# Optimization experiments

Hardware: AMD Instinct MI355X
Metric: run time of the kernel (lower is better)

## Reference

```python
import jax, jax.numpy as jnp
import numpy as np

# (dx, dy) per TL_table order: lower_right, down, lower_left, right, left, upper_right, up, upper_left
DIRS = [(1, 1), (0, 1), (-1, 1), (1, 0), (-1, 0), (1, -1), (0, -1), (-1, -1)]


def shift(x, dr, dc, pad=0.0):
    # result[r, c] = x[r - dr, c - dc]; out-of-range filled with `pad`.
    B, R, C = x.shape
    pr = (dr, 0) if dr >= 0 else (0, -dr)
    pc = (dc, 0) if dc >= 0 else (0, -dc)
    y = jnp.pad(x, ((0, 0), pr, pc), constant_values=pad)
    r0 = 0 if dr >= 0 else -dr
    c0 = 0 if dc >= 0 else -dc
    return y[:, r0:r0 + R, c0:c0 + C]


def conn_mask_gen(mask, K):
    m = mask[:, 0]  # [B, R, C]
    # conn[i] = mask * mask shifted by K pixels in direction DIRS[i]
    return jnp.stack([m * shift(m, K * dy, K * dx) for (dx, dy) in DIRS], axis=1)


def get_zero_one_mask(mask, K):
    inv = 1.0 - mask[:, 0]  # [B, R, C]
    inv_static = jnp.broadcast_to(inv[:, None], (inv.shape[0], 8) + inv.shape[1:])
    # inverse_direction_mask is initialized to ONES -> shift with pad=1, reversed direction
    inv_dir = jnp.stack([shift(inv, -K * dy, -K * dx, pad=1.0) for (dx, dy) in DIRS], axis=1)
    return inv_static * (1.0 - inv_static * inv_dir)


def pair_loss(c_map, conn_mask, K, positive):
    c = c_map[:, 0]  # [B, R, C]
    p1 = conn_mask * c[:, None]  # [B, 8, R, C]
    # p2[i] = (conn_mask[7-i] * c) shifted K pixels in direction DIRS[i]
    p2 = jnp.stack([shift(conn_mask[:, 7 - i] * c, K * dy, K * dx)
                    for i, (dx, dy) in enumerate(DIRS)], axis=1)
    pp = p1 * p2
    if positive:
        term1 = conn_mask * (-jnp.log(p2 + 1e-4) - jnp.log(p1 + 1e-4))
        term2 = conn_mask * (-jnp.log(pp + 1e-4) + jnp.exp(-pp))
    else:
        term1 = conn_mask * (-jnp.log(1.0 - p2 + 1e-4) - jnp.log(1.0 - p1 + 1e-4))
        term2 = conn_mask * (-jnp.log(1.0 - pp + 1e-4) + jnp.exp(-pp))
    return conn_mask * term1 / (term2 + 1e-5)


def neighbor_loss(c_map, target, T1, T2, K):
    zom = get_zero_one_mask(target, K)  # [B, 8, R, C]
    c = c_map[:, 0]
    p2 = jnp.stack([shift(zom[:, i] * c, K * dy, K * dx)
                    for i, (dx, dy) in enumerate(DIRS)], axis=1)
    p1m = jnp.stack([shift(zom[:, i], K * dy, K * dx)
                     for i, (dx, dy) in enumerate(DIRS)], axis=1)
    p1 = p1m * c[:, None]
    term1 = -T1 * p1m * jnp.log(1.0 - p2 + 1e-4) - T2 * p1m * jnp.log(p1 + 1e-5)
    term2 = -p1m * jnp.log(1.0 - p1 * p2 + 1e-4) + p1m * jnp.exp(-p2)
    return (p1m * term1 / (term2 + 1e-5)).mean()


def sc_loss(c_map, target_f):
    c = jax.nn.sigmoid(c_map)
    nb1 = neighbor_loss(c, target_f, 0.8, 0.2, K=1)
    nb2 = neighbor_loss(c, target_f, 0.8, 0.2, K=2)
    n1 = pair_loss(c, conn_mask_gen(1.0 - target_f, 1), 1, positive=False)
    n2 = pair_loss(c, conn_mask_gen(1.0 - target_f, 2), 2, positive=False)
    p1 = pair_loss(c, conn_mask_gen(target_f, 1), 1, positive=True)
    p2 = pair_loss(c, conn_mask_gen(target_f, 2), 2, positive=True)
    loss = 0.7 * (n1 + 0.5 * n2) + 0.3 * (p1 + 0.5 * p2) + 0.7 * (0.5 * nb1 + 0.5 * nb2)
    return loss.mean()


def setup_inputs() -> dict:
    key = jax.random.key(0)
    k1, k2 = jax.random.split(key)
    B, H, W = 8, 512, 512
    c_map = jax.random.normal(k1, (B, 1, H, W), dtype=jnp.float32)
    target = jax.random.randint(k2, (B, 1, H, W), 0, 2, dtype=jnp.int32)
    return {"c_map": c_map, "target": target}


def reference(c_map, target):
    return sc_loss(c_map, target.astype(jnp.float32))
```

## Files before the change

kernel.cpp:

```cpp
#include <hip/hip_runtime.h>

#define IMG_H 512
#define IMG_W 512
#define NB    8
#define TILE  32
#define LROWS 34
#define LCOLS 36
#define NBLK  (NB * (IMG_H / TILE) * (IMG_W / TILE))
#define N_MEAN 16777216.0
#define LOG2E 1.44269504f
#define LN2   0.69314718f

__device__ __forceinline__ float frcp(float x){ return __builtin_amdgcn_rcpf(x); }
__device__ __forceinline__ float fexp2(float x){ return __builtin_amdgcn_exp2f(x); }
__device__ __forceinline__ float flog2(float x){ return __builtin_amdgcn_logf(x); }

__global__ __launch_bounds__(256) void scloss_main(
    const float* __restrict__ cmap, const int* __restrict__ tgt,
    float* __restrict__ partials)
{
    __shared__ float4 pack[LROWS * LCOLS];

    const int tilesPerRow = IMG_W / TILE;
    const int tilesPerImg = (IMG_H / TILE) * tilesPerRow;
    int blk = blockIdx.x;
    int b   = blk / tilesPerImg;
    int ti  = blk % tilesPerImg;
    int tr  = (ti / tilesPerRow) * TILE;
    int tc  = (ti % tilesPerRow) * TILE;

    const float* cimg = cmap + (size_t)b * (IMG_H * IMG_W);
    const int*   timg = tgt  + (size_t)b * (IMG_H * IMG_W);

    for (int idx = threadIdx.x; idx < LROWS * LCOLS; idx += 256) {
        int lr = idx / LCOLS, lc = idx - lr * LCOLS;
        int gr = tr + lr, gc = tc + lc - 2;
        float4 v = make_float4(0.0f, 0.0f, 0.0f, 0.0f);
        if (gr < IMG_H && (unsigned)gc < (unsigned)IMG_W) {
            float x = cimg[gr * IMG_W + gc];
            bool  t = timg[gr * IMG_W + gc] != 0;
            float s   = frcp(1.0f + fexp2(x * -LOG2E));
            float sel = t ? s : (1.0f - s);
            float L   = LN2 * flog2(sel + 1e-4f);
            float e   = fexp2(s * -LOG2E);
            v = make_float4(s,
                            (t ? -0.6f : -1.4f) * L,
                            t ? -e : e,
                            (t ? -0.07f : -0.28f) * L);
        }
        pack[idx] = v;
    }
    __syncthreads();

    int j  = threadIdx.x & 31;
    int i0 = threadIdx.x >> 5;
    float acc = 0.0f;

#define EDGE(VBX, Dd, Nn, WSK, MK) do {                                   \
        float4 vb  = (VBX);                                               \
        bool  tb   = vb.z < 0.0f;                                         \
        bool  qpos = (ta == tb);                  \
        bool  qnz  = vb.z != 0.0f;                \
        float ppp  = __builtin_fmaf(sa, vb.x, 1e-4f);                     \
        float ompp = __builtin_fmaf(-sa, vb.x, 1.0001f);                  \
        float argc = (qpos && ta) ? ppp : ompp;                           \
        float lg   = flog2(argc);                                         \
        float E    = fexp2(__builtin_fmaf(ppp, -LOG2E, 1e-4f * LOG2E));   \
        float een  = ta ? vb.z : epa;         \
        float ee   = qpos ? E : een;                                      \
        Dd         = __builtin_fmaf(-LN2, lg, ee);                        \
        float nm   = qpos ? __builtin_fmaf(WSK, vb.y, MK) : (nwa + vb.w); \
        Nn         = qnz ? nm : 0.0f;                                     \
    } while (0)

#define COMBINE do {                                                      \
        float d01 = D0 * D1, d23 = D2 * D3;                               \
        float R   = frcp(d01 * d23);                                      \
        float n01 = __builtin_fmaf(N1, D0, N0 * D1);                      \
        float n23 = __builtin_fmaf(N3, D2, N2 * D3);                      \
        acc = __builtin_fmaf(__builtin_fmaf(n23, d01, n01 * d23), R, acc);\
    } while (0)

#define PIXEL(VA, S1X, S2X, base) do {                                    \
        float4 va_ = (VA);                                                \
        bool  ta  = va_.z < 0.0f;                                         \
        float sa  = va_.x, nwa = va_.w, epa = va_.z;                      \
        float mwa = va_.y, hmw = 0.5f * va_.y;                            \
        float D0, D1, D2, D3, N0, N1, N2, N3;                             \
        EDGE(base[1],           D0, N0, 1.0f, mwa);            \
        EDGE(base[LCOLS + 1],   D1, N1, 1.0f, mwa);            \
        EDGE(S1X,               D2, N2, 1.0f, mwa);            \
        EDGE(base[LCOLS - 1],   D3, N3, 1.0f, mwa);            \
        COMBINE;                                                          \
        EDGE(base[2],           D0, N0, 0.5f, hmw);            \
        EDGE(base[2*LCOLS + 2], D1, N1, 0.5f, hmw);            \
        EDGE(S2X,               D2, N2, 0.5f, hmw);            \
        EDGE(base[2*LCOLS - 2], D3, N3, 0.5f, hmw);            \
        COMBINE;                                                          \
    } while (0)

    {
        const float4* b0 = &pack[(i0 * 4) * LCOLS + (j + 2)];
        const float4* b1 = b0 + LCOLS;
        const float4* b2 = b1 + LCOLS;
        const float4* b3 = b2 + LCOLS;
        float4 va0 = b0[0], va1 = b1[0], va2 = b2[0], va3 = b3[0];
        PIXEL(va0, va1, va2,            b0);
        PIXEL(va1, va2, va3,            b1);
        PIXEL(va2, va3, b2[2 * LCOLS],  b2);
        PIXEL(va3, b3[LCOLS], b3[2 * LCOLS], b3);
    }
#undef PIXEL
#undef COMBINE
#undef EDGE

    #pragma unroll
    for (int o = 32; o > 0; o >>= 1) acc += __shfl_down(acc, o, 64);
    __shared__ float wsum[4];
    int lane = threadIdx.x & 63, wid = threadIdx.x >> 6;
    if (lane == 0) wsum[wid] = acc;
    __syncthreads();
    if (threadIdx.x == 0)
        partials[blockIdx.x] = wsum[0] + wsum[1] + wsum[2] + wsum[3];
}

__global__ __launch_bounds__(256) void scloss_final(
    const float* __restrict__ partials, int n, float* __restrict__ out)
{
    double a = 0.0;
    for (int i = threadIdx.x; i < n; i += 256) a += (double)partials[i];
    __shared__ double sd[256];
    sd[threadIdx.x] = a;
    __syncthreads();
    for (int s = 128; s > 0; s >>= 1) {
        if (threadIdx.x < s) sd[threadIdx.x] += sd[threadIdx.x + s];
        __syncthreads();
    }
    if (threadIdx.x == 0) out[0] = (float)(sd[0] / N_MEAN);
}

extern "C" void kernel_launch(void* const* d_in, const int* in_sizes, int n_in,
                              void* d_out, int out_size, void* d_ws, size_t ws_size,
                              hipStream_t stream) {
    const float* cmap = (const float*)d_in[0];
    const int*   tgt  = (const int*)d_in[1];
    float* out      = (float*)d_out;
    float* partials = (float*)d_ws;

    scloss_main<<<NBLK, 256, 0, stream>>>(cmap, tgt, partials);
    scloss_final<<<1, 256, 0, stream>>>(partials, NBLK, out);
}
```

Baseline: 24.48 us.

## Halve tile height to 16x32, unroll halo load, raise occupancy hint

Switches tiles from 32x32 to 16x32, so each thread computes 2 pixels instead of 4 and the grid doubles in block count. The halo-loading loop is replaced by three explicitly unrolled, predicated loads that issue their global reads before any transcendental work, and launch bounds request 8 blocks per CU. The aim is more parallelism and better latency hiding, at the cost of a larger halo-recompute fraction (18 rows loaded per 16 computed) and twice as many partial sums.

```diff
diff --git a/kernel.cpp b/kernel.cpp
--- a/kernel.cpp
+++ b/kernel.cpp
@@ -3,10 +3,14 @@
 #define IMG_H 512
 #define IMG_W 512
 #define NB    8
-#define TILE  32
-#define LROWS 34
-#define LCOLS 36
-#define NBLK  (NB * (IMG_H / TILE) * (IMG_W / TILE))
+#define TILE_R 16
+#define TILE_C 32
+#define LROWS (TILE_R + 2)
+#define LCOLS (TILE_C + 4)
+#define NELEM (LROWS * LCOLS)
+#define TPR   (IMG_W / TILE_C)
+#define TPI   ((IMG_H / TILE_R) * TPR)
+#define NBLK  (NB * TPI)
 #define N_MEAN 16777216.0
 #define LOG2E 1.44269504f
 #define LN2   0.69314718f
@@ -15,40 +19,52 @@
 __device__ __forceinline__ float fexp2(float x){ return __builtin_amdgcn_exp2f(x); }
 __device__ __forceinline__ float flog2(float x){ return __builtin_amdgcn_logf(x); }
 
-__global__ __launch_bounds__(256) void scloss_main(
+__device__ __forceinline__ float4 make_pack(float x, int t_, bool ok) {
+    if (!ok) return make_float4(0.0f, 0.0f, 0.0f, 0.0f);
+    bool  t = t_ != 0;
+    float s   = frcp(1.0f + fexp2(x * -LOG2E));
+    float sel = t ? s : (1.0f - s);
+    float L   = LN2 * flog2(sel + 1e-4f);
+    float e   = fexp2(s * -LOG2E);
+    return make_float4(s, (t ? -0.6f : -1.4f) * L, t ? -e : e,
+                       (t ? -0.07f : -0.28f) * L);
+}
+
+__global__ __launch_bounds__(256, 8) void scloss_main(
     const float* __restrict__ cmap, const int* __restrict__ tgt,
     float* __restrict__ partials)
 {
-    __shared__ float4 pack[LROWS * LCOLS];
+    __shared__ float4 pack[NELEM];
 
-    const int tilesPerRow = IMG_W / TILE;
-    const int tilesPerImg = (IMG_H / TILE) * tilesPerRow;
     int blk = blockIdx.x;
-    int b   = blk / tilesPerImg;
-    int ti  = blk % tilesPerImg;
-    int tr  = (ti / tilesPerRow) * TILE;
-    int tc  = (ti % tilesPerRow) * TILE;
+    int b   = blk / TPI;
+    int ti  = blk % TPI;
+    int tr  = (ti / TPR) * TILE_R;
+    int tc  = (ti % TPR) * TILE_C;
 
     const float* cimg = cmap + (size_t)b * (IMG_H * IMG_W);
     const int*   timg = tgt  + (size_t)b * (IMG_H * IMG_W);
 
-    for (int idx = threadIdx.x; idx < LROWS * LCOLS; idx += 256) {
-        int lr = idx / LCOLS, lc = idx - lr * LCOLS;
-        int gr = tr + lr, gc = tc + lc - 2;
-        float4 v = make_float4(0.0f, 0.0f, 0.0f, 0.0f);
-        if (gr < IMG_H && (unsigned)gc < (unsigned)IMG_W) {
-            float x = cimg[gr * IMG_W + gc];
-            bool  t = timg[gr * IMG_W + gc] != 0;
-            float s   = frcp(1.0f + fexp2(x * -LOG2E));
-            float sel = t ? s : (1.0f - s);
-            float L   = LN2 * flog2(sel + 1e-4f);
-            float e   = fexp2(s * -LOG2E);
-            v = make_float4(s,
-                            (t ? -0.6f : -1.4f) * L,
-                            t ? -e : e,
-                            (t ? -0.07f : -0.28f) * L);
-        }
-        pack[idx] = v;
+    {
+        const int idx0 = threadIdx.x, idx1 = idx0 + 256, idx2 = idx0 + 512;
+        int lr0 = idx0 / LCOLS, lc0 = idx0 - lr0 * LCOLS;
+        int lr1 = idx1 / LCOLS, lc1 = idx1 - lr1 * LCOLS;
+        int lr2 = idx2 / LCOLS, lc2 = idx2 - lr2 * LCOLS;
+        int gr0 = tr + lr0, gc0 = tc + lc0 - 2;
+        int gr1 = tr + lr1, gc1 = tc + lc1 - 2;
+        int gr2 = tr + lr2, gc2 = tc + lc2 - 2;
+        bool ok0 = (gr0 < IMG_H) && ((unsigned)gc0 < (unsigned)IMG_W);
+        bool ok1 = (gr1 < IMG_H) && ((unsigned)gc1 < (unsigned)IMG_W);
+        bool in2 = idx2 < NELEM;
+        bool ok2 = in2 && (gr2 < IMG_H) && ((unsigned)gc2 < (unsigned)IMG_W);
+        float c0 = 0.0f, c1 = 0.0f, c2 = 0.0f;
+        int   t0 = 0,    t1 = 0,    t2 = 0;
+        if (ok0) { int o = gr0 * IMG_W + gc0; c0 = cimg[o]; t0 = timg[o]; }
+        if (ok1) { int o = gr1 * IMG_W + gc1; c1 = cimg[o]; t1 = timg[o]; }
+        if (ok2) { int o = gr2 * IMG_W + gc2; c2 = cimg[o]; t2 = timg[o]; }
+        pack[idx0] = make_pack(c0, t0, ok0);
+        pack[idx1] = make_pack(c1, t1, ok1);
+        if (in2) pack[idx2] = make_pack(c2, t2, ok2);
     }
     __syncthreads();
 
@@ -56,8 +72,8 @@
     int i0 = threadIdx.x >> 5;
     float acc = 0.0f;
 
-#define EDGE(VBX, Dd, Nn, WSK, MK) do {                                   \
-        float4 vb  = (VBX);                                               \
+#define EDGE(VB, Dd, Nn, WSK, MK) do {                                    \
+        float4 vb  = (VB);                                                \
         bool  tb   = vb.z < 0.0f;                                         \
         bool  qpos = (ta == tb);                  \
         bool  qnz  = vb.z != 0.0f;                \
@@ -82,7 +98,7 @@
     } while (0)
 
 #define PIXEL(VA, S1X, S2X, base) do {                                    \
-        float4 va_ = (VA);                                                \
+        float4 va_  = (VA);                                               \
         bool  ta  = va_.z < 0.0f;                                         \
         float sa  = va_.x, nwa = va_.w, epa = va_.z;                      \
         float mwa = va_.y, hmw = 0.5f * va_.y;                            \
@@ -100,15 +116,11 @@
     } while (0)
 
     {
-        const float4* b0 = &pack[(i0 * 4) * LCOLS + (j + 2)];
+        const float4* b0 = &pack[(2 * i0) * LCOLS + (j + 2)];
         const float4* b1 = b0 + LCOLS;
-        const float4* b2 = b1 + LCOLS;
-        const float4* b3 = b2 + LCOLS;
-        float4 va0 = b0[0], va1 = b1[0], va2 = b2[0], va3 = b3[0];
-        PIXEL(va0, va1, va2,            b0);
-        PIXEL(va1, va2, va3,            b1);
-        PIXEL(va2, va3, b2[2 * LCOLS],  b2);
-        PIXEL(va3, b3[LCOLS], b3[2 * LCOLS], b3);
+        float4 va0 = b0[0], va1 = b1[0];
+        PIXEL(va0, va1, b0[2 * LCOLS], b0);
+        PIXEL(va1, b1[LCOLS], b1[2 * LCOLS], b1);
     }
 #undef PIXEL
 #undef COMBINE
```

After: 25.87 us. +5.7%, slower.
